# Performance work log

Hardware: AMD Instinct MI355X
Metric: run time of the kernel (lower is better)

Reference implementation:

```python
import jax, jax.numpy as jnp
import numpy as np

L, D, H, F = 2, 512, 8, 2048
B, S = 1, 2048
DH = D // H
EPS = 1e-6
NEG = -1e9


def setup_inputs() -> dict:
    key = jax.random.key(0)
    ks = jax.random.split(key, 8)
    s = 0.02
    return {
        "x": jax.random.normal(ks[0], (B, S, D), jnp.float32),
        "enc_output": jax.random.normal(ks[1], (B, S, D), jnp.float32),
        # per-layer stacked params; axis 1 of attn weights = [wq, wk, wv, wo]
        "attn1_w": jax.random.normal(ks[2], (L, 4, D, D), jnp.float32) * s,
        "attn1_b": jnp.zeros((L, 4, D), jnp.float32),
        "attn2_w": jax.random.normal(ks[3], (L, 4, D, D), jnp.float32) * s,
        "attn2_b": jnp.zeros((L, 4, D), jnp.float32),
        "ffn_w1": jax.random.normal(ks[4], (L, D, F), jnp.float32) * s,
        "ffn_b1": jnp.zeros((L, F), jnp.float32),
        "ffn_w2": jax.random.normal(ks[5], (L, F, D), jnp.float32) * s,
        "ffn_b2": jnp.zeros((L, D), jnp.float32),
        # axis 1 = [norm1, norm2, norm3]
        "ln_g": jnp.ones((L, 3, D), jnp.float32),
        "ln_b": jnp.zeros((L, 3, D), jnp.float32),
    }


def positional_encoding(seq_len, num_feat):
    pos = jnp.arange(seq_len, dtype=jnp.float32)[:, None]
    dims = jnp.arange(num_feat, dtype=jnp.float32)[None, :]
    rates = 1.0 / jnp.power(10000.0, 2.0 * jnp.floor(dims / 2.0) / num_feat)
    ang = pos * rates  # [S, D]
    # keras module concatenates sines(even cols) and cosines(odd cols)
    return jnp.concatenate([jnp.sin(ang[:, 0::2]), jnp.cos(ang[:, 1::2])], axis=-1)[None]


def layer_norm(x, g, b):
    mu = jnp.mean(x, axis=-1, keepdims=True)
    var = jnp.mean(jnp.square(x - mu), axis=-1, keepdims=True)
    return (x - mu) * jax.lax.rsqrt(var + EPS) * g + b


def split_heads(x):
    b, s, _ = x.shape
    return x.reshape(b, s, H, DH).transpose(0, 2, 1, 3)  # [B,H,S,dh]


def mha(q_in, k_in, v_in, w, bias, mask):
    q = split_heads(q_in @ w[0] + bias[0])
    k = split_heads(k_in @ w[1] + bias[1])
    v = split_heads(v_in @ w[2] + bias[2])
    logits = jnp.einsum("bhqd,bhkd->bhqk", q, k) / jnp.sqrt(jnp.float32(DH))
    if mask is not None:
        logits = logits + mask * NEG
    weights = jax.nn.softmax(logits, axis=-1)
    out = jnp.einsum("bhqk,bhkd->bhqd", weights, v)
    b, _, s, _ = out.shape
    out = out.transpose(0, 2, 1, 3).reshape(b, s, D)
    return out @ w[3] + bias[3]


def decoder_forward(x, enc_output, attn1_w, attn1_b, attn2_w, attn2_b,
                    ffn_w1, ffn_b1, ffn_w2, ffn_b2, ln_g, ln_b):
    s = x.shape[1]
    x = x + positional_encoding(s, x.shape[2])
    causal = jnp.triu(jnp.ones((s, s), jnp.float32), k=1)[None, None]  # 1 = masked

    def layer(x, p):
        a1w, a1b, a2w, a2b, w1, b1, w2, b2, g, bn = p
        attn1 = mha(x, x, x, a1w, a1b, causal)
        x = layer_norm(x + attn1, g[0], bn[0])
        attn2 = mha(x, enc_output, enc_output, a2w, a2b, None)
        x = layer_norm(x + attn2, g[1], bn[1])
        ffn = jax.nn.relu(x @ w1 + b1) @ w2 + b2
        x = layer_norm(x + ffn, g[2], bn[2])
        return x, None

    x, _ = jax.lax.scan(layer, x, (attn1_w, attn1_b, attn2_w, attn2_b,
                                   ffn_w1, ffn_b1, ffn_w2, ffn_b2, ln_g, ln_b))
    return x


def reference(x, enc_output, attn1_w, attn1_b, attn2_w, attn2_b,
              ffn_w1, ffn_b1, ffn_w2, ffn_b2, ln_g, ln_b):
    return decoder_forward(x, enc_output, attn1_w, attn1_b, attn2_w, attn2_b,
                           ffn_w1, ffn_b1, ffn_w2, ffn_b2, ln_g, ln_b)
```

## Files before the change

kernel.cpp:

```cpp
#include <hip/hip_runtime.h>
#include <hip/hip_bf16.h>
#include <math.h>

#define S 2048
#define D 512
#define H 8
#define DH 64
#define F 2048
#define NLAYER 2

typedef __attribute__((ext_vector_type(8))) short bf16x8;
typedef __attribute__((ext_vector_type(4))) float f32x4;
typedef __hip_bfloat16 bf16;

typedef __attribute__((address_space(3))) unsigned int lds_u32;
typedef __attribute__((address_space(1))) const unsigned int glb_u32;

__device__ __forceinline__ void gld16(const void* g, void* l) {
    __builtin_amdgcn_global_load_lds((glb_u32*)g, (lds_u32*)l, 16, 0, 0);
}

__global__ __launch_bounds__(256)
void prep_all(const float* __restrict__ a1w, const float* __restrict__ a2w,
              const float* __restrict__ fw1, const float* __restrict__ fw2,
              bf16* __restrict__ wts,
              const float* __restrict__ x, const float* __restrict__ enc,
              float* __restrict__ xbF, bf16* __restrict__ xbB,
              bf16* __restrict__ encB)
{
    const size_t WCH = 1048576;
    const size_t DD = (size_t)D * D, DF = (size_t)D * F;
    __shared__ float t[64][65];
    const int b = blockIdx.x;
    const int tid = threadIdx.x;

    if (b < 2048) {
        const float* src;
        bf16* dst;
        int R, C, xt, yt;
        if (b < 1024) {
            int m = b >> 6, tt = b & 63;
            xt = tt & 7; yt = tt >> 3;
            R = D; C = D;
            if (m < 8) { src = a1w + (size_t)m * DD; dst = wts + (size_t)(m >> 2) * WCH + (size_t)(m & 3) * DD; }
            else { int m2 = m - 8; src = a2w + (size_t)m2 * DD; dst = wts + 2 * WCH + (size_t)(m2 >> 2) * WCH + (size_t)(m2 & 3) * DD; }
        } else if (b < 1536) {
            int tt = b - 1024;
            int m = tt >> 8; tt &= 255;
            xt = tt & 7; yt = tt >> 3;
            R = D; C = F;
            src = fw1 + (size_t)m * DF; dst = wts + (size_t)(4 + m) * WCH;
        } else {
            int tt = b - 1536;
            int m = tt >> 8; tt &= 255;
            xt = tt & 31; yt = tt >> 5;
            R = F; C = D;
            src = fw2 + (size_t)m * DF; dst = wts + (size_t)(6 + m) * WCH;
        }
        const int rb = xt * 64, cb = yt * 64;
        for (int i = tid; i < 4096; i += 256) {
            int r = i >> 6, c = i & 63;
            t[r][c] = src[(size_t)(rb + r) * C + cb + c];
        }
        __syncthreads();
        for (int i = tid; i < 4096; i += 256) {
            int r = i >> 6, c = i & 63;
            dst[(size_t)(cb + r) * R + rb + c] = __float2bfloat16(t[c][r]);
        }
    } else {
        int idx = (b - 2048) * 256 + tid;
        if (idx < S * D) {
            int s = idx / D;
            int j = idx % D;
            int jj = (j < D / 2) ? j : j - D / 2;
            float rate = expf(-(float)jj * (logf(10000.0f) / (float)(D / 2)));
            float ang = (float)s * rate;
            float pe = (j < D / 2) ? sinf(ang) : cosf(ang);
            float v = x[idx] + pe;
            xbF[idx] = v;
            xbB[idx] = __float2bfloat16(v);
            encB[idx] = __float2bfloat16(enc[idx]);
        }
    }
}

template<int BM, int BN, int BK, int MODE>
__global__ __launch_bounds__(256)
void gemm_bf16(const bf16* __restrict__ A, const bf16* __restrict__ Aalt,
               const bf16* __restrict__ Bt,
               const float* __restrict__ bias, float* __restrict__ outF,
               bf16* __restrict__ outB, int K, int ldc, int relu,
               bf16* __restrict__ q16, bf16* __restrict__ kh,
               bf16* __restrict__ vt, int qn, int kn)
{
    constexpr int MI = BM / 32, NJ = BN / 32;
    constexpr int SL = BK / 8;
    constexpr int KS = BK / 32;
    constexpr int HALF = (BM + BN) * BK * 2;
    constexpr int IA = BM * SL / 256, IB = BN * SL / 256;
    constexpr int TS = BN + 8;
    constexpr int LDS_VB = (MODE == 1) ? BM * TS * 2 : 0;
    constexpr int LDSZ = (2 * HALF > LDS_VB) ? 2 * HALF : LDS_VB;
    __shared__ char lds[LDSZ];
    const int tid = threadIdx.x;
    const int w = tid >> 6, l = tid & 63;
    const int l15 = l & 15, l4 = l >> 4;
    const int bm = blockIdx.y * BM, bn = blockIdx.x * BN;
    const int wr = (w >> 1) * (BM / 2), wc = (w & 1) * (BN / 2);
    const bf16* Ause = (MODE == 1 && bn >= qn) ? Aalt : A;

    f32x4 acc[MI][NJ] = {};

#define XV(row) ((BK == 64) ? ((row) & 7) : (((row) >> 1) & 3))
#define GSTAGE(k0, b)                                                          \
    {                                                                          \
        _Pragma("unroll")                                                      \
        for (int i = 0; i < IA; ++i) {                                         \
            int n = (w * IA + i) * 64 + l;                                     \
            int row = n / SL;                                                  \
            int sl = (n % SL) ^ XV(row);                                       \
            gld16(Ause + (size_t)(bm + row) * K + (k0) + sl * 8,               \
                  lds + (b) * HALF + (w * IA + i) * 1024);                     \
        }                                                                      \
        _Pragma("unroll")                                                      \
        for (int i = 0; i < IB; ++i) {                                         \
            int n = (w * IB + i) * 64 + l;                                     \
            int row = n / SL;                                                  \
            int sl = (n % SL) ^ XV(row);                                       \
            gld16(Bt + (size_t)(bn + row) * K + (k0) + sl * 8,                 \
                  lds + (b) * HALF + BM * BK * 2 + (w * IB + i) * 1024);       \
        }                                                                      \
    }

    GSTAGE(0, 0);
    __syncthreads();
    int cur = 0;
    for (int k0 = 0; k0 < K; k0 += BK) {
        if (k0 + BK < K) GSTAGE(k0 + BK, cur ^ 1);
        const char* base = lds + cur * HALF;
        bf16x8 af[MI][KS], bfr[NJ][KS];
#pragma unroll
        for (int i = 0; i < MI; ++i) {
            int row = wr + i * 16 + l15;
#pragma unroll
            for (int s = 0; s < KS; ++s)
                af[i][s] = *(const bf16x8*)(base + row * (BK * 2)
                                            + (((s * 4 + l4) ^ XV(row)) << 4));
        }
#pragma unroll
        for (int j = 0; j < NJ; ++j) {
            int row = wc + j * 16 + l15;
#pragma unroll
            for (int s = 0; s < KS; ++s)
                bfr[j][s] = *(const bf16x8*)(base + BM * BK * 2 + row * (BK * 2)
                                             + (((s * 4 + l4) ^ XV(row)) << 4));
        }
#pragma unroll
        for (int s = 0; s < KS; ++s)
#pragma unroll
            for (int i = 0; i < MI; ++i)
#pragma unroll
                for (int j = 0; j < NJ; ++j)
                    acc[i][j] = __builtin_amdgcn_mfma_f32_16x16x32_bf16(af[i][s], bfr[j][s], acc[i][j], 0, 0, 0);
        __syncthreads();
        cur ^= 1;
    }
#undef GSTAGE
#undef XV

    if (MODE == 0) {
#pragma unroll
        for (int i = 0; i < MI; ++i)
#pragma unroll
            for (int j = 0; j < NJ; ++j)
#pragma unroll
                for (int q = 0; q < 4; ++q) {
                    int row = bm + wr + i * 16 + l4 * 4 + q;
                    int col = bn + wc + j * 16 + l15;
                    float v = acc[i][j][q] + bias[col];
                    if (relu) v = fmaxf(v, 0.f);
                    if (outF) outF[(size_t)row * ldc + col] = v;
                    if (outB) outB[(size_t)row * ldc + col] = __float2bfloat16(v);
                }
    } else {
        const int creg = (bn < qn) ? 0 : (bn < qn + kn ? 1 : 2);
        if (creg < 2) {
#pragma unroll
            for (int i = 0; i < MI; ++i)
#pragma unroll
                for (int j = 0; j < NJ; ++j)
#pragma unroll
                    for (int q = 0; q < 4; ++q) {
                        int row = bm + wr + i * 16 + l4 * 4 + q;
                        int col = bn + wc + j * 16 + l15;
                        float v = acc[i][j][q] + bias[col];
                        if (creg == 0) {
                            q16[(size_t)row * 512 + col] = __float2bfloat16(v);
                        } else {
                            int c2 = col - qn;
                            kh[((size_t)(c2 >> 6) * S + row) * 64 + (c2 & 63)] = __float2bfloat16(v);
                        }
                    }
        } else {
            short* t = (short*)lds;
#pragma unroll
            for (int i = 0; i < MI; ++i)
#pragma unroll
                for (int j = 0; j < NJ; ++j)
#pragma unroll
                    for (int q = 0; q < 4; ++q) {
                        int r = wr + i * 16 + l4 * 4 + q;
                        int c = wc + j * 16 + l15;
                        float v = acc[i][j][q] + bias[bn + c];
                        t[r * TS + c] = __builtin_bit_cast(short, __float2bfloat16(v));
                    }
            __syncthreads();
            const int dgb = bn - qn - kn;
            constexpr int SGR = BM / 8;
            for (int i2 = tid; i2 < BN * SGR; i2 += 256) {
                int dl = i2 / SGR;
                int s8 = (i2 % SGR) * 8;
                bf16x8 v;
#pragma unroll
                for (int jj = 0; jj < 8; ++jj)
                    v[jj] = t[(s8 + jj) * TS + dl];
                *(bf16x8*)(vt + (size_t)(dgb + dl) * S + bm + s8) = v;
            }
        }
    }
}

template<int CAUSAL>
__global__ __launch_bounds__(512)
void attn_mfma7(const bf16* __restrict__ Q, const bf16* __restrict__ Kh,
                const bf16* __restrict__ Vt, bf16* __restrict__ O)
{
    __shared__ char lds[82944];
    const int tid = threadIdx.x;
    const int w = tid >> 6, l = tid & 63;
    const int l15 = l & 15, l4 = l >> 4;
    const int g = w >> 2, wl = w & 3;
    const int h = blockIdx.x, qb = blockIdx.y;
    const int qw = qb * 64 + wl * 16;
    const int qr = qw + l15;
    char* plds = lds + 65536 + w * 2048;

    const float QSC = 0.1803368801f;
    bf16x8 aq[2];
#pragma unroll
    for (int s = 0; s < 2; ++s) {
        bf16x8 raw = *(const bf16x8*)(Q + (size_t)(qw + l15) * 512 + h * DH + s * 32 + l4 * 8);
#pragma unroll
        for (int j = 0; j < 8; ++j) {
            float f = __builtin_bit_cast(float, ((unsigned int)(unsigned short)raw[j]) << 16) * QSC;
            raw[j] = __builtin_bit_cast(short, __float2bfloat16(f));
        }
        aq[s] = raw;
    }

    f32x4 o[4] = {};
    float mrun = -1e30f, lrun = 0.f;
    const int cmax = CAUSAL ? qb : (S / 64 - 1);
    const int nits = cmax / 2 + 1;

#define STAGE(ii, p)                                                                \
    {                                                                               \
        const int cc = 2 * (ii) + g;                                                \
        if (cc <= cmax) {                                                           \
            const int kb2 = cc * 64;                                                \
            _Pragma("unroll")                                                       \
            for (int i = 0; i < 2; ++i) {                                           \
                int n = wl * 128 + i * 64 + l;                                      \
                int row = n >> 3;                                                   \
                int sl = (n & 7) ^ (row & 7);                                       \
                gld16(Kh + ((size_t)h * S + kb2 + row) * 64 + sl * 8,               \
                      lds + (p) * 32768 + g * 16384 + wl * 2048 + i * 1024);        \
                gld16(Vt + ((size_t)(h * 64 + row)) * S + kb2 + sl * 8,             \
                      lds + (p) * 32768 + g * 16384 + 8192 + wl * 2048 + i * 1024); \
            }                                                                       \
        }                                                                           \
    }

    STAGE(0, 0);
    __syncthreads();

    int cur = 0;
    for (int it = 0; it < nits; ++it) {
        if (it + 1 < nits) STAGE(it + 1, cur ^ 1);
        const int c = 2 * it + g;
        if (c <= cmax) {
            const char* kb = lds + cur * 32768 + g * 16384;
            const char* vb = kb + 8192;
            const int kbase = c * 64;

            f32x4 st[4];
            __builtin_amdgcn_s_setprio(1);
#pragma unroll
            for (int t = 0; t < 4; ++t) {
                f32x4 sacc = {0.f, 0.f, 0.f, 0.f};
#pragma unroll
                for (int s = 0; s < 2; ++s) {
                    bf16x8 kf = *(const bf16x8*)(kb + (t * 16 + l15) * 128
                                                 + (((s * 4 + l4) ^ (l15 & 7)) << 4));
                    sacc = __builtin_amdgcn_mfma_f32_16x16x32_bf16(kf, aq[s], sacc, 0, 0, 0);
                }
                st[t] = sacc;
            }
            __builtin_amdgcn_s_setprio(0);

            float mx = -1e30f;
#pragma unroll
            for (int t = 0; t < 4; ++t)
#pragma unroll
                for (int r = 0; r < 4; ++r) {
                    float v = st[t][r];
                    if (CAUSAL && c == cmax) {
                        int key = kbase + t * 16 + l4 * 4 + r;
                        if (key > qr) v = -1e30f;
                    }
                    st[t][r] = v;
                    mx = fmaxf(mx, v);
                }
            mx = fmaxf(mx, __shfl_xor(mx, 16));
            mx = fmaxf(mx, __shfl_xor(mx, 32));

            if (__any(mx > mrun + 8.0f)) {
                float mnew = fmaxf(mrun, mx);
                float scl = exp2f(mrun - mnew);
                mrun = mnew;
                lrun *= scl;
#pragma unroll
                for (int j = 0; j < 4; ++j) {
                    float sj = __shfl(scl, (l & 48) | (l4 * 4 + j));
#pragma unroll
                    for (int dt = 0; dt < 4; ++dt) o[dt][j] *= sj;
                }
            }

            float ps = 0.f;
#pragma unroll
            for (int t = 0; t < 4; ++t) {
                float e0 = exp2f(st[t][0] - mrun);
                float e1 = exp2f(st[t][1] - mrun);
                float e2 = exp2f(st[t][2] - mrun);
                float e3 = exp2f(st[t][3] - mrun);
                ps += (e0 + e1) + (e2 + e3);
                unsigned int lo = (unsigned int)(unsigned short)__builtin_bit_cast(short, __float2bfloat16(e0))
                                | ((unsigned int)(unsigned short)__builtin_bit_cast(short, __float2bfloat16(e1)) << 16);
                unsigned int hi = (unsigned int)(unsigned short)__builtin_bit_cast(short, __float2bfloat16(e2))
                                | ((unsigned int)(unsigned short)__builtin_bit_cast(short, __float2bfloat16(e3)) << 16);
                uint2 pk; pk.x = lo; pk.y = hi;
                int byte = (l15 * 128 + t * 32 + l4 * 8) ^ ((l15 & 7) << 4);
                *(uint2*)(plds + byte) = pk;
            }
            ps += __shfl_xor(ps, 16);
            ps += __shfl_xor(ps, 32);
            lrun += ps;

            bf16x8 pf[2];
#pragma unroll
            for (int s = 0; s < 2; ++s) {
                int byte = (l15 * 128 + s * 64 + l4 * 16) ^ ((l15 & 7) << 4);
                pf[s] = *(const bf16x8*)(plds + byte);
            }
            __builtin_amdgcn_s_setprio(1);
#pragma unroll
            for (int dt = 0; dt < 4; ++dt)
#pragma unroll
                for (int s = 0; s < 2; ++s) {
                    bf16x8 vf = *(const bf16x8*)(vb + (dt * 16 + l15) * 128
                                                 + (((s * 4 + l4) ^ (l15 & 7)) << 4));
                    o[dt] = __builtin_amdgcn_mfma_f32_16x16x32_bf16(pf[s], vf, o[dt], 0, 0, 0);
                }
            __builtin_amdgcn_s_setprio(0);
        }
        __syncthreads();
        cur ^= 1;
    }
#undef STAGE

#pragma unroll
    for (int dt = 0; dt < 4; ++dt)
#pragma unroll
        for (int j = 0; j < 4; ++j) {
            int q = l4 * 4 + j;
            int d = dt * 16 + l15;
            int byte = q * 128 + ((d * 2) ^ ((q & 7) << 4));
            *(short*)(plds + byte) = __builtin_bit_cast(short, __float2bfloat16(o[dt][j]));
        }
    if (l < 16) {
        *(float*)(lds + 81920 + w * 128 + l * 8) = mrun;
        *(float*)(lds + 81920 + w * 128 + l * 8 + 4) = lrun;
    }
    __syncthreads();

    {
        const int qt16 = tid >> 7;
        const int idx = tid & 127;
        const int q = idx >> 3;
        const int d0 = (idx & 7) * 8;
        const char* p0 = lds + 65536 + qt16 * 2048;
        const char* p1 = lds + 65536 + (qt16 + 4) * 2048;
        float m0 = *(const float*)(lds + 81920 + qt16 * 128 + q * 8);
        float l0 = *(const float*)(lds + 81920 + qt16 * 128 + q * 8 + 4);
        float m1 = *(const float*)(lds + 81920 + (qt16 + 4) * 128 + q * 8);
        float l1 = *(const float*)(lds + 81920 + (qt16 + 4) * 128 + q * 8 + 4);
        float mt = fmaxf(m0, m1);
        float f0 = exp2f(m0 - mt), f1 = exp2f(m1 - mt);
        float lt = f0 * l0 + f1 * l1;
        float inv = 1.f / lt;
        int byte = q * 128 + ((d0 * 2) ^ ((q & 7) << 4));
        bf16x8 a = *(const bf16x8*)(p0 + byte);
        bf16x8 b = *(const bf16x8*)(p1 + byte);
        bf16x8 r;
#pragma unroll
        for (int jj = 0; jj < 8; ++jj) {
            float va = __builtin_bit_cast(float, ((unsigned int)(unsigned short)a[jj]) << 16);
            float vb2 = __builtin_bit_cast(float, ((unsigned int)(unsigned short)b[jj]) << 16);
            r[jj] = __builtin_bit_cast(short, __float2bfloat16((f0 * va + f1 * vb2) * inv));
        }
        *(bf16x8*)(O + (size_t)(qb * 64 + qt16 * 16 + q) * D + h * DH + d0) = r;
    }
}

__global__ __launch_bounds__(128)
void add_ln_kernel(const float* __restrict__ a, const float* __restrict__ b,
                   const float* __restrict__ g, const float* __restrict__ beta,
                   float* __restrict__ outF, bf16* __restrict__ outB)
{
    const int row = blockIdx.x;
    const int tid = threadIdx.x;
    float4 av = *(const float4*)&a[(size_t)row * D + tid * 4];
    float4 bv = *(const float4*)&b[(size_t)row * D + tid * 4];
    float4 s;
    s.x = av.x + bv.x; s.y = av.y + bv.y; s.z = av.z + bv.z; s.w = av.w + bv.w;
    float sum = s.x + s.y + s.z + s.w;
    float sq = s.x * s.x + s.y * s.y + s.z * s.z + s.w * s.w;
#pragma unroll
    for (int off = 32; off > 0; off >>= 1) {
        sum += __shfl_xor(sum, off);
        sq  += __shfl_xor(sq, off);
    }
    __shared__ float red[4];
    if ((tid & 63) == 0) { red[(tid >> 6) * 2] = sum; red[(tid >> 6) * 2 + 1] = sq; }
    __syncthreads();
    sum = red[0] + red[2];
    sq  = red[1] + red[3];
    float mu = sum / (float)D;
    float var = sq / (float)D - mu * mu;
    float rs = rsqrtf(var + 1e-6f);
    float4 gv = *(const float4*)&g[tid * 4];
    float4 bt = *(const float4*)&beta[tid * 4];
    float4 o;
    o.x = (s.x - mu) * rs * gv.x + bt.x;
    o.y = (s.y - mu) * rs * gv.y + bt.y;
    o.z = (s.z - mu) * rs * gv.z + bt.z;
    o.w = (s.w - mu) * rs * gv.w + bt.w;
    *(float4*)&outF[(size_t)row * D + tid * 4] = o;
    if (outB) {
        outB[(size_t)row * D + tid * 4 + 0] = __float2bfloat16(o.x);
        outB[(size_t)row * D + tid * 4 + 1] = __float2bfloat16(o.y);
        outB[(size_t)row * D + tid * 4 + 2] = __float2bfloat16(o.z);
        outB[(size_t)row * D + tid * 4 + 3] = __float2bfloat16(o.w);
    }
}

extern "C" void kernel_launch(void* const* d_in, const int* in_sizes, int n_in,
                              void* d_out, int out_size, void* d_ws, size_t ws_size,
                              hipStream_t stream)
{
    const float* x   = (const float*)d_in[0];
    const float* enc = (const float*)d_in[1];
    const float* a1w = (const float*)d_in[2];
    const float* a1b = (const float*)d_in[3];
    const float* a2w = (const float*)d_in[4];
    const float* a2b = (const float*)d_in[5];
    const float* fw1 = (const float*)d_in[6];
    const float* fb1 = (const float*)d_in[7];
    const float* fw2 = (const float*)d_in[8];
    const float* fb2 = (const float*)d_in[9];
    const float* lng = (const float*)d_in[10];
    const float* lnb = (const float*)d_in[11];
    float* out = (float*)d_out;

    char* wsb = (char*)d_ws;
    float* xb   = (float*)(wsb);
    float* ao   = (float*)(wsb + ((size_t)4 << 20));
    bf16* xb16  = (bf16*)(wsb + ((size_t)8 << 20));
    bf16* enc16 = (bf16*)(wsb + ((size_t)10 << 20));
    bf16* att16 = (bf16*)(wsb + ((size_t)12 << 20));
    bf16* q16   = (bf16*)(wsb + ((size_t)14 << 20));
    bf16* kh16  = (bf16*)(wsb + ((size_t)16 << 20));
    bf16* vt16  = (bf16*)(wsb + ((size_t)18 << 20));
    bf16* ffh16 = att16;
    bf16* wts   = (bf16*)(wsb + ((size_t)20 << 20));
    const size_t WCH = 1048576;
    const size_t DD = (size_t)D * D;

    prep_all<<<6144, 256, 0, stream>>>(a1w, a2w, fw1, fw2, wts, x, enc, xb, xb16, enc16);

    for (int l = 0; l < NLAYER; ++l) {
        const bf16* A1T = wts + (size_t)(0 + l) * WCH;
        const bf16* A2T = wts + (size_t)(2 + l) * WCH;
        const bf16* W1T = wts + (size_t)(4 + l) * WCH;
        const bf16* W2T = wts + (size_t)(6 + l) * WCH;
        const float* b1v = a1b + (size_t)l * 4 * D;
        const float* b2v = a2b + (size_t)l * 4 * D;

        gemm_bf16<64, 64, 64, 1><<<dim3(24, 32), 256, 0, stream>>>(
            xb16, xb16, A1T, b1v, nullptr, nullptr, D, 0, 0, q16, kh16, vt16, 512, 512);
        attn_mfma7<1><<<dim3(H, S / 64), 512, 0, stream>>>(q16, kh16, vt16, att16);
        gemm_bf16<32, 64, 64, 0><<<dim3(8, 64), 256, 0, stream>>>(
            att16, att16, A1T + 3 * DD, b1v + 3 * D, ao, nullptr, D, D, 0, nullptr, nullptr, nullptr, 0, 0);
        add_ln_kernel<<<S, 128, 0, stream>>>(xb, ao, lng + (size_t)(l * 3 + 0) * D, lnb + (size_t)(l * 3 + 0) * D, xb, xb16);

        gemm_bf16<64, 64, 64, 1><<<dim3(24, 32), 256, 0, stream>>>(
            xb16, enc16, A2T, b2v, nullptr, nullptr, D, 0, 0, q16, kh16, vt16, 512, 512);
        attn_mfma7<0><<<dim3(H, S / 64), 512, 0, stream>>>(q16, kh16, vt16, att16);
        gemm_bf16<32, 64, 64, 0><<<dim3(8, 64), 256, 0, stream>>>(
            att16, att16, A2T + 3 * DD, b2v + 3 * D, ao, nullptr, D, D, 0, nullptr, nullptr, nullptr, 0, 0);
        add_ln_kernel<<<S, 128, 0, stream>>>(xb, ao, lng + (size_t)(l * 3 + 1) * D, lnb + (size_t)(l * 3 + 1) * D, xb, xb16);

        gemm_bf16<64, 64, 64, 0><<<dim3(32, 32), 256, 0, stream>>>(
            xb16, xb16, W1T, fb1 + (size_t)l * F, nullptr, ffh16, D, F, 1, nullptr, nullptr, nullptr, 0, 0);
        gemm_bf16<32, 64, 64, 0><<<dim3(8, 64), 256, 0, stream>>>(
            ffh16, ffh16, W2T, fb2 + (size_t)l * D, ao, nullptr, F, D, 0, nullptr, nullptr, nullptr, 0, 0);
        float* dstF = (l == NLAYER - 1) ? out : xb;
        bf16* dstB = (l == NLAYER - 1) ? nullptr : xb16;
        add_ln_kernel<<<S, 128, 0, stream>>>(xb, ao, lng + (size_t)(l * 3 + 2) * D, lnb + (size_t)(l * 3 + 2) * D, dstF, dstB);
    }
}
```

Before: 266.6 us.

## Fuse residual add and LayerNorm into output-projection GEMM epilogues via cross-block reduction

Adds a GEMM epilogue mode that adds bias and residual, computes per-row partial sums and sums of squares, and combines them across the 8 column blocks of each row tile with global atomics. A spin-wait counter acts as the barrier before normalizing and writing fp32 and bf16 outputs. This removes six separate add+LayerNorm launches and the fp32 intermediate buffer round-trip. In exchange it relies on all column blocks of a row tile being co-resident, otherwise the spin-wait can deadlock. It also adds atomic traffic and a memset of the scratch counters on every call.

```diff
diff --git a/kernel.cpp b/kernel.cpp
--- a/kernel.cpp
+++ b/kernel.cpp
@@ -91,7 +91,10 @@
                const float* __restrict__ bias, float* __restrict__ outF,
                bf16* __restrict__ outB, int K, int ldc, int relu,
                bf16* __restrict__ q16, bf16* __restrict__ kh,
-               bf16* __restrict__ vt, int qn, int kn)
+               bf16* __restrict__ vt, int qn, int kn,
+               const float* __restrict__ xbIn, const float* __restrict__ lgam,
+               const float* __restrict__ lbet, float* __restrict__ rsumG,
+               float* __restrict__ rsqG, unsigned int* __restrict__ cntG)
 {
     constexpr int MI = BM / 32, NJ = BN / 32;
     constexpr int SL = BK / 8;
@@ -182,7 +185,7 @@
                     if (outF) outF[(size_t)row * ldc + col] = v;
                     if (outB) outB[(size_t)row * ldc + col] = __float2bfloat16(v);
                 }
-    } else {
+    } else if (MODE == 1) {
         const int creg = (bn < qn) ? 0 : (bn < qn + kn ? 1 : 2);
         if (creg < 2) {
 #pragma unroll
@@ -227,6 +230,76 @@
                 *(bf16x8*)(vt + (size_t)(dgb + dl) * S + bm + s8) = v;
             }
         }
+    } else {
+        float s_[NJ][4];
+        float psum[4], psq[4];
+#pragma unroll
+        for (int q = 0; q < 4; ++q) { psum[q] = 0.f; psq[q] = 0.f; }
+#pragma unroll
+        for (int j = 0; j < NJ; ++j)
+#pragma unroll
+            for (int q = 0; q < 4; ++q) {
+                int row = bm + wr + l4 * 4 + q;
+                int col = bn + wc + j * 16 + l15;
+                float v = acc[0][j][q] + bias[col] + xbIn[(size_t)row * 512 + col];
+                s_[j][q] = v;
+                psum[q] += v;
+                psq[q] += v * v;
+            }
+#pragma unroll
+        for (int q = 0; q < 4; ++q)
+#pragma unroll
+            for (int off = 1; off < 16; off <<= 1) {
+                psum[q] += __shfl_xor(psum[q], off);
+                psq[q]  += __shfl_xor(psq[q], off);
+            }
+        float* lsum = (float*)lds;
+        float* lsq  = (float*)(lds + 256);
+        float* lmu  = (float*)(lds + 512);
+        float* lrsv = (float*)(lds + 640);
+        if (l15 == 0) {
+#pragma unroll
+            for (int q = 0; q < 4; ++q) {
+                int rl = wr + l4 * 4 + q;
+                lsum[rl * 2 + (w & 1)] = psum[q];
+                lsq [rl * 2 + (w & 1)] = psq[q];
+            }
+        }
+        __syncthreads();
+        if (tid < 32) {
+            float bs = lsum[tid * 2] + lsum[tid * 2 + 1];
+            float bq = lsq [tid * 2] + lsq [tid * 2 + 1];
+            atomicAdd(&rsumG[blockIdx.y * 32 + tid], bs);
+            atomicAdd(&rsqG [blockIdx.y * 32 + tid], bq);
+        }
+        __threadfence();
+        __syncthreads();
+        if (tid == 0) {
+            atomicAdd(&cntG[blockIdx.y], 1u);
+            while (atomicAdd(&cntG[blockIdx.y], 0u) < 8u)
+                __builtin_amdgcn_s_sleep(8);
+        }
+        __syncthreads();
+        if (tid < 32) {
+            float ts = atomicAdd(&rsumG[blockIdx.y * 32 + tid], 0.f);
+            float tq = atomicAdd(&rsqG [blockIdx.y * 32 + tid], 0.f);
+            float mu = ts * (1.f / 512.f);
+            float var = tq * (1.f / 512.f) - mu * mu;
+            lmu[tid] = mu;
+            lrsv[tid] = rsqrtf(var + 1e-6f);
+        }
+        __syncthreads();
+#pragma unroll
+        for (int j = 0; j < NJ; ++j)
+#pragma unroll
+            for (int q = 0; q < 4; ++q) {
+                int rl = wr + l4 * 4 + q;
+                int row = bm + rl;
+                int col = bn + wc + j * 16 + l15;
+                float ov = (s_[j][q] - lmu[rl]) * lrsv[rl] * lgam[col] + lbet[col];
+                outF[(size_t)row * ldc + col] = ov;
+                if (outB) outB[(size_t)row * ldc + col] = __float2bfloat16(ov);
+            }
     }
 }
 
@@ -423,48 +496,6 @@
     }
 }
 
-__global__ __launch_bounds__(128)
-void add_ln_kernel(const float* __restrict__ a, const float* __restrict__ b,
-                   const float* __restrict__ g, const float* __restrict__ beta,
-                   float* __restrict__ outF, bf16* __restrict__ outB)
-{
-    const int row = blockIdx.x;
-    const int tid = threadIdx.x;
-    float4 av = *(const float4*)&a[(size_t)row * D + tid * 4];
-    float4 bv = *(const float4*)&b[(size_t)row * D + tid * 4];
-    float4 s;
-    s.x = av.x + bv.x; s.y = av.y + bv.y; s.z = av.z + bv.z; s.w = av.w + bv.w;
-    float sum = s.x + s.y + s.z + s.w;
-    float sq = s.x * s.x + s.y * s.y + s.z * s.z + s.w * s.w;
-#pragma unroll
-    for (int off = 32; off > 0; off >>= 1) {
-        sum += __shfl_xor(sum, off);
-        sq  += __shfl_xor(sq, off);
-    }
-    __shared__ float red[4];
-    if ((tid & 63) == 0) { red[(tid >> 6) * 2] = sum; red[(tid >> 6) * 2 + 1] = sq; }
-    __syncthreads();
-    sum = red[0] + red[2];
-    sq  = red[1] + red[3];
-    float mu = sum / (float)D;
-    float var = sq / (float)D - mu * mu;
-    float rs = rsqrtf(var + 1e-6f);
-    float4 gv = *(const float4*)&g[tid * 4];
-    float4 bt = *(const float4*)&beta[tid * 4];
-    float4 o;
-    o.x = (s.x - mu) * rs * gv.x + bt.x;
-    o.y = (s.y - mu) * rs * gv.y + bt.y;
-    o.z = (s.z - mu) * rs * gv.z + bt.z;
-    o.w = (s.w - mu) * rs * gv.w + bt.w;
-    *(float4*)&outF[(size_t)row * D + tid * 4] = o;
-    if (outB) {
-        outB[(size_t)row * D + tid * 4 + 0] = __float2bfloat16(o.x);
-        outB[(size_t)row * D + tid * 4 + 1] = __float2bfloat16(o.y);
-        outB[(size_t)row * D + tid * 4 + 2] = __float2bfloat16(o.z);
-        outB[(size_t)row * D + tid * 4 + 3] = __float2bfloat16(o.w);
-    }
-}
-
 extern "C" void kernel_launch(void* const* d_in, const int* in_sizes, int n_in,
                               void* d_out, int out_size, void* d_ws, size_t ws_size,
                               hipStream_t stream)
@@ -485,7 +516,6 @@
 
     char* wsb = (char*)d_ws;
     float* xb   = (float*)(wsb);
-    float* ao   = (float*)(wsb + ((size_t)4 << 20));
     bf16* xb16  = (bf16*)(wsb + ((size_t)8 << 20));
     bf16* enc16 = (bf16*)(wsb + ((size_t)10 << 20));
     bf16* att16 = (bf16*)(wsb + ((size_t)12 << 20));
@@ -494,8 +524,11 @@
     bf16* vt16  = (bf16*)(wsb + ((size_t)18 << 20));
     bf16* ffh16 = att16;
     bf16* wts   = (bf16*)(wsb + ((size_t)20 << 20));
+    char* lnsc  = wsb + ((size_t)36 << 20);
     const size_t WCH = 1048576;
     const size_t DD = (size_t)D * D;
+
+    hipMemsetAsync(lnsc, 0, 6 * 32768, stream);
 
     prep_all<<<6144, 256, 0, stream>>>(a1w, a2w, fw1, fw2, wts, x, enc, xb, xb16, enc16);
 
@@ -507,26 +540,38 @@
         const float* b1v = a1b + (size_t)l * 4 * D;
         const float* b2v = a2b + (size_t)l * 4 * D;
 
+#define LNSCRATCH(k) (float*)(lnsc + (size_t)(l * 3 + (k)) * 32768),              \
+                     (float*)(lnsc + (size_t)(l * 3 + (k)) * 32768 + 8192),       \
+                     (unsigned int*)(lnsc + (size_t)(l * 3 + (k)) * 32768 + 16384)
+
         gemm_bf16<64, 64, 64, 1><<<dim3(24, 32), 256, 0, stream>>>(
-            xb16, xb16, A1T, b1v, nullptr, nullptr, D, 0, 0, q16, kh16, vt16, 512, 512);
+            xb16, xb16, A1T, b1v, nullptr, nullptr, D, 0, 0, q16, kh16, vt16, 512, 512,
+            nullptr, nullptr, nullptr, nullptr, nullptr, nullptr);
         attn_mfma7<1><<<dim3(H, S / 64), 512, 0, stream>>>(q16, kh16, vt16, att16);
-        gemm_bf16<32, 64, 64, 0><<<dim3(8, 64), 256, 0, stream>>>(
-            att16, att16, A1T + 3 * DD, b1v + 3 * D, ao, nullptr, D, D, 0, nullptr, nullptr, nullptr, 0, 0);
-        add_ln_kernel<<<S, 128, 0, stream>>>(xb, ao, lng + (size_t)(l * 3 + 0) * D, lnb + (size_t)(l * 3 + 0) * D, xb, xb16);
+        gemm_bf16<32, 64, 64, 2><<<dim3(8, 64), 256, 0, stream>>>(
+            att16, att16, A1T + 3 * DD, b1v + 3 * D, xb, xb16, D, D, 0,
+            nullptr, nullptr, nullptr, 0, 0,
+            xb, lng + (size_t)(l * 3 + 0) * D, lnb + (size_t)(l * 3 + 0) * D, LNSCRATCH(0));
 
         gemm_bf16<64, 64, 64, 1><<<dim3(24, 32), 256, 0, stream>>>(
-            xb16, enc16, A2T, b2v, nullptr, nullptr, D, 0, 0, q16, kh16, vt16, 512, 512);
+            xb16, enc16, A2T, b2v, nullptr, nullptr, D, 0, 0, q16, kh16, vt16, 512, 512,
+            nullptr, nullptr, nullptr, nullptr, nullptr, nullptr);
         attn_mfma7<0><<<dim3(H, S / 64), 512, 0, stream>>>(q16, kh16, vt16, att16);
-        gemm_bf16<32, 64, 64, 0><<<dim3(8, 64), 256, 0, stream>>>(
-            att16, att16, A2T + 3 * DD, b2v + 3 * D, ao, nullptr, D, D, 0, nullptr, nullptr, nullptr, 0, 0);
-        add_ln_kernel<<<S, 128, 0, stream>>>(xb, ao, lng + (size_t)(l * 3 + 1) * D, lnb + (size_t)(l * 3 + 1) * D, xb, xb16);
+        gemm_bf16<32, 64, 64, 2><<<dim3(8, 64), 256, 0, stream>>>(
+            att16, att16, A2T + 3 * DD, b2v + 3 * D, xb, xb16, D, D, 0,
+            nullptr, nullptr, nullptr, 0, 0,
+            xb, lng + (size_t)(l * 3 + 1) * D, lnb + (size_t)(l * 3 + 1) * D, LNSCRATCH(1));
 
         gemm_bf16<64, 64, 64, 0><<<dim3(32, 32), 256, 0, stream>>>(
-            xb16, xb16, W1T, fb1 + (size_t)l * F, nullptr, ffh16, D, F, 1, nullptr, nullptr, nullptr, 0, 0);
-        gemm_bf16<32, 64, 64, 0><<<dim3(8, 64), 256, 0, stream>>>(
-            ffh16, ffh16, W2T, fb2 + (size_t)l * D, ao, nullptr, F, D, 0, nullptr, nullptr, nullptr, 0, 0);
+            xb16, xb16, W1T, fb1 + (size_t)l * F, nullptr, ffh16, D, F, 1,
+            nullptr, nullptr, nullptr, 0, 0,
+            nullptr, nullptr, nullptr, nullptr, nullptr, nullptr);
         float* dstF = (l == NLAYER - 1) ? out : xb;
         bf16* dstB = (l == NLAYER - 1) ? nullptr : xb16;
-        add_ln_kernel<<<S, 128, 0, stream>>>(xb, ao, lng + (size_t)(l * 3 + 2) * D, lnb + (size_t)(l * 3 + 2) * D, dstF, dstB);
+        gemm_bf16<32, 64, 64, 2><<<dim3(8, 64), 256, 0, stream>>>(
+            ffh16, ffh16, W2T, fb2 + (size_t)l * D, dstF, dstB, F, D, 0,
+            nullptr, nullptr, nullptr, 0, 0,
+            xb, lng + (size_t)(l * 3 + 2) * D, lnb + (size_t)(l * 3 + 2) * D, LNSCRATCH(2));
+#undef LNSCRATCH
     }
 }
```

Result: slower. 492.1 us (+84.6%).
